# Kernel optimization log

Measured on AMD Instinct MI355X. Metric: run time of the kernel, lower is better.

Reference implementation:

```python
import jax, jax.numpy as jnp
import numpy as np

WS = 8        # window_size
SHIFT = 4     # shift_size
NH = 6        # num_heads
EPS = 1e-5


def _rel_pos_index(ws):
    coords = np.stack(np.meshgrid(np.arange(ws), np.arange(ws), indexing='ij'))  # [2,ws,ws]
    cf = coords.reshape(2, -1)                      # [2, ws*ws]
    rel = cf[:, :, None] - cf[:, None, :]           # [2, N, N]
    rel = rel.transpose(1, 2, 0)                    # [N, N, 2]
    rel[:, :, 0] += ws - 1
    rel[:, :, 1] += ws - 1
    rel[:, :, 0] *= 2 * ws - 1
    return rel.sum(-1)                              # [N, N] int


def _attn_mask(H, W, ws, shift):
    img = np.zeros((H, W), dtype=np.float32)
    slices = (slice(0, -ws), slice(-ws, -shift), slice(-shift, None))
    cnt = 0
    for hs in slices:
        for wsl in slices:
            img[hs, wsl] = cnt
            cnt += 1
    mw = img.reshape(H // ws, ws, W // ws, ws).transpose(0, 2, 1, 3).reshape(-1, ws * ws)
    diff = mw[:, None, :] - mw[:, :, None]          # [nW, N, N]
    return np.where(diff != 0, -100.0, 0.0).astype(np.float32)


def _layernorm(x, g, b):
    mu = x.mean(-1, keepdims=True)
    var = ((x - mu) ** 2).mean(-1, keepdims=True)
    return (x - mu) * jax.lax.rsqrt(var + EPS) * g + b


def setup_inputs() -> dict:
    key = jax.random.key(0)
    ks = jax.random.split(key, 8)
    C, HID = 192, 768
    return {
        'x': jax.random.normal(ks[0], (8, 128, 128, C), jnp.float32),
        'g1': jnp.ones((C,), jnp.float32),
        'b1': jnp.zeros((C,), jnp.float32),
        'qkv_w': jax.random.normal(ks[1], (3 * C, C), jnp.float32) * 0.02,
        'qkv_b': jnp.zeros((3 * C,), jnp.float32),
        'rpb_table': jax.random.normal(ks[2], ((2 * WS - 1) ** 2, NH), jnp.float32) * 0.02,
        'proj_w': jax.random.normal(ks[3], (C, C), jnp.float32) * 0.02,
        'proj_b': jnp.zeros((C,), jnp.float32),
        'g2': jnp.ones((C,), jnp.float32),
        'b2': jnp.zeros((C,), jnp.float32),
        'fc1_w': jax.random.normal(ks[4], (HID, C), jnp.float32) * 0.02,
        'fc1_b': jnp.zeros((HID,), jnp.float32),
        'fc2_w': jax.random.normal(ks[5], (C, HID), jnp.float32) * 0.02,
        'fc2_b': jnp.zeros((C,), jnp.float32),
    }


def reference(x, g1, b1, qkv_w, qkv_b, rpb_table, proj_w, proj_b, g2, b2,
              fc1_w, fc1_b, fc2_w, fc2_b):
    B, H, W, C = x.shape
    N = WS * WS
    hd = C // NH
    scale = hd ** -0.5

    rpi = jnp.asarray(_rel_pos_index(WS))                 # [N,N] static
    mask = jnp.asarray(_attn_mask(H, W, WS, SHIFT))       # [nW,N,N] static
    nW = mask.shape[0]

    shortcut = x.reshape(B, H * W, C)
    xn = _layernorm(shortcut, g1, b1).reshape(B, H, W, C)

    # cyclic shift
    xs = jnp.roll(xn, shift=(-SHIFT, -SHIFT), axis=(1, 2))

    # window partition -> [B*nW, N, C]
    win = xs.reshape(B, H // WS, WS, W // WS, WS, C).transpose(0, 1, 3, 2, 4, 5)
    win = win.reshape(-1, N, C)
    B_ = win.shape[0]

    # qkv
    qkv = jnp.einsum('bnc,oc->bno', win, qkv_w) + qkv_b   # [B_,N,3C]
    qkv = qkv.reshape(B_, N, 3, NH, hd).transpose(2, 0, 3, 1, 4)  # [3,B_,NH,N,hd]
    q, k, v = qkv[0] * scale, qkv[1], qkv[2]

    attn = jnp.einsum('bhnd,bhmd->bhnm', q, k)            # [B_,NH,N,N]
    bias = rpb_table[rpi.reshape(-1)].reshape(N, N, NH).transpose(2, 0, 1)
    attn = attn + bias[None]
    attn = attn.reshape(B, nW, NH, N, N) + mask[None, :, None]
    attn = jax.nn.softmax(attn.reshape(B_, NH, N, N), axis=-1)

    out = jnp.einsum('bhnm,bhmd->bhnd', attn, v)          # [B_,NH,N,hd]
    out = out.transpose(0, 2, 1, 3).reshape(B_, N, C)
    out = jnp.einsum('bnc,oc->bno', out, proj_w) + proj_b

    # window reverse -> [B,H,W,C]
    out = out.reshape(B, H // WS, W // WS, WS, WS, C).transpose(0, 1, 3, 2, 4, 5)
    out = out.reshape(B, H, W, C)
    out = jnp.roll(out, shift=(SHIFT, SHIFT), axis=(1, 2)).reshape(B, H * W, C)

    x1 = shortcut + out
    h = _layernorm(x1, g2, b2)
    h = jnp.einsum('bnc,hc->bnh', h, fc1_w) + fc1_b
    h = jax.nn.gelu(h, approximate=False)
    h = jnp.einsum('bnh,ch->bnc', h, fc2_w) + fc2_b
    x2 = x1 + h
    return x2.reshape(B, H, W, C)
```

## Files before the change

### kernel.cpp

```cpp
#include <hip/hip_runtime.h>
#include <hip/hip_bf16.h>

typedef __attribute__((ext_vector_type(8))) short s16x8;
typedef __attribute__((ext_vector_type(4))) float f32x4;

__device__ __forceinline__ unsigned short f2bf(float f){
    __hip_bfloat16 h = __float2bfloat16(f);
    return *reinterpret_cast<unsigned short*>(&h);
}

__device__ __forceinline__ int flab(int g){ return (g < 120) ? 0 : ((g < 124) ? 1 : 2); }

__device__ __forceinline__ void async16(const void* g, void* l){
    __builtin_amdgcn_global_load_lds(
        (const __attribute__((address_space(1))) unsigned int*)g,
        (__attribute__((address_space(3))) unsigned int*)l, 16, 0, 0);
}

__global__ __launch_bounds__(256) void wconv_all(
    const float* __restrict__ w0, const float* __restrict__ w1,
    const float* __restrict__ w2, const float* __restrict__ w3,
    unsigned short* __restrict__ o0, unsigned short* __restrict__ o1,
    unsigned short* __restrict__ o2, unsigned short* __restrict__ o3)
{
    int i = blockIdx.x*256 + threadIdx.x;
    if (i < 110592) o0[i] = f2bf(w0[i]);
    if (i < 36864)  o1[i] = f2bf(w1[i]);
    if (i < 147456) {
        int o = i/192, k = i - o*192;
        int oc = o/192, r = o - oc*192, ks = k>>5, c = k&31;
        o2[((oc*6 + ks)*192 + r)*32 + c] = f2bf(w2[i]);
    }
    if (i < 147456) {
        int o = i/768, k = i - o*768;
        int q = o/48, r = o - q*48, ks = k>>5, c = k&31;
        o3[((q*24 + ks)*48 + r)*32 + c] = f2bf(w3[i]);
    }
}

__global__ __launch_bounds__(256) void lnqkv_kernel(
    const float* __restrict__ x, const float* __restrict__ g1, const float* __restrict__ b1,
    const unsigned short* __restrict__ wq, const float* __restrict__ qkvb,
    unsigned short* __restrict__ qo, unsigned short* __restrict__ ko,
    unsigned short* __restrict__ vo)
{
    __shared__ __attribute__((aligned(16))) unsigned short win[64*200];
    __shared__ __attribute__((aligned(16))) unsigned short Bs[64*200];
    const int b_ = blockIdx.x;
    const int bb = b_>>8, wi = b_&255, wh = wi>>4, ww = wi&15;
    const int tid = threadIdx.x;
    const int wv = tid>>6, lane = tid&63, lrow = lane&15, quad = lane>>4;

    {
        const int n = tid>>2, q4 = tid&3;
        const int r = n>>3, c = n&7;
        const int hh = (wh*8 + r + 4)&127, wp = (ww*8 + c + 4)&127;
        const float* px = x + (((size_t)bb*128+hh)*128+wp)*192 + q4*48;
        float v[48];
        #pragma unroll
        for (int m=0;m<12;++m) *(float4*)(v+m*4) = *(const float4*)(px+m*4);
        float s = 0.f;
        #pragma unroll
        for (int k=0;k<48;++k) s += v[k];
        s += __shfl_xor(s,1); s += __shfl_xor(s,2);
        float mu = s*(1.0f/192.0f);
        float qv = 0.f;
        #pragma unroll
        for (int k=0;k<48;++k){ float d=v[k]-mu; qv += d*d; }
        qv += __shfl_xor(qv,1); qv += __shfl_xor(qv,2);
        float rstd = rsqrtf(qv*(1.0f/192.0f) + 1e-5f);
        const float* pg = g1 + q4*48;
        const float* pb = b1 + q4*48;
        unsigned short* pw = win + n*200 + q4*48;
        #pragma unroll
        for (int k=0;k<48;++k) pw[k] = f2bf((v[k]-mu)*rstd*pg[k] + pb[k]);
    }
    __syncthreads();

    s16x8 af[6];
    #pragma unroll
    for (int kc=0;kc<6;++kc)
        af[kc] = *(const s16x8*)(win + (wv*16+lrow)*200 + kc*32 + quad*8);

    for (int ot=0; ot<9; ++ot) {
        const int o0 = ot*64;
        __syncthreads();
        #pragma unroll
        for (int t=0;t<6;++t) {
            int cid = tid + t*256;
            *(int4*)(Bs + (cid/24)*200 + (cid%24)*8) =
                *(const int4*)(wq + (size_t)o0*192 + cid*8);
        }
        __syncthreads();
        f32x4 acc[4];
        #pragma unroll
        for (int j=0;j<4;++j) acc[j] = (f32x4){0.f,0.f,0.f,0.f};
        #pragma unroll
        for (int kc=0;kc<6;++kc)
            #pragma unroll
            for (int j=0;j<4;++j) {
                s16x8 bf = *(const s16x8*)(Bs + (j*16+lrow)*200 + kc*32 + quad*8);
                acc[j] = __builtin_amdgcn_mfma_f32_16x16x32_bf16(af[kc], bf, acc[j], 0, 0, 0);
            }
        __syncthreads();
        unsigned short* T = Bs;
        const int part = ot/3;
        float bv[4];
        #pragma unroll
        for (int j=0;j<4;++j) bv[j] = qkvb[o0 + j*16 + lrow];

        if (part < 2) {
            const float scale = (part==0) ? 0.17677669529663687f : 1.0f;
            #pragma unroll
            for (int j=0;j<4;++j)
                #pragma unroll
                for (int rg=0;rg<4;++rg) {
                    int n2 = wv*16 + quad*4 + rg;
                    T[n2*72 + j*16 + lrow] = f2bf((acc[j][rg]+bv[j])*scale);
                }
            __syncthreads();
            unsigned short* dst = (part==0) ? qo : ko;
            #pragma unroll
            for (int t=0;t<2;++t) {
                int c = tid + t*256;
                int n2 = c>>3, blk = c&7;
                int o_in = o0 + blk*8 - part*192;
                int head = o_in>>5, d = o_in&31;
                *(int4*)(dst + (((size_t)b_*6+head)*64 + n2)*32 + d) =
                    *(const int4*)(T + n2*72 + blk*8);
            }
        } else {
            #pragma unroll
            for (int j=0;j<4;++j)
                #pragma unroll
                for (int rg=0;rg<4;++rg) {
                    int n2 = wv*16 + quad*4 + rg;
                    T[(j*16+lrow)*72 + n2] = f2bf(acc[j][rg]+bv[j]);
                }
            __syncthreads();
            #pragma unroll
            for (int t=0;t<2;++t) {
                int c = tid + t*256;
                int ol = c>>3, nb = (c&7)*8;
                int o_in = o0 + ol - 384;
                int head = o_in>>5, d = o_in&31;
                *(int4*)(vo + (((size_t)b_*6+head)*32 + d)*64 + nb) =
                    *(const int4*)(T + ol*72 + nb);
            }
        }
    }
}

__global__ __launch_bounds__(384) void attn_kernel(
    const unsigned short* __restrict__ q, const unsigned short* __restrict__ k,
    const unsigned short* __restrict__ vT, const float* __restrict__ rpb,
    unsigned short* __restrict__ ao)
{
    __shared__ float rpb_s[1350];
    __shared__ __attribute__((aligned(16))) unsigned short p_lds[6*4608];
    const int b_ = blockIdx.x;
    const int h = threadIdx.x >> 6;
    const int lane = threadIdx.x & 63, lrow = lane & 15, quad = lane >> 4;
    for (int i = threadIdx.x; i < 1350; i += 384) rpb_s[i] = rpb[i];
    __syncthreads();

    const size_t hb = ((size_t)b_*6 + h)*2048;
    const unsigned short* qb = q  + hb;
    const unsigned short* kb = k  + hb;
    const unsigned short* vb = vT + hb;

    s16x8 qf[4], kf[4];
    #pragma unroll
    for (int i = 0; i < 4; ++i) qf[i] = *(const s16x8*)(qb + (i*16+lrow)*32 + quad*8);
    #pragma unroll
    for (int j = 0; j < 4; ++j) kf[j] = *(const s16x8*)(kb + (j*16+lrow)*32 + quad*8);

    const f32x4 zz = {0.f,0.f,0.f,0.f};
    f32x4 s[4][4];
    #pragma unroll
    for (int i = 0; i < 4; ++i)
        #pragma unroll
        for (int j = 0; j < 4; ++j)
            s[i][j] = __builtin_amdgcn_mfma_f32_16x16x32_bf16(qf[i], kf[j], zz, 0, 0, 0);

    const int wi = b_ & 255, wh = wi >> 4, ww = wi & 15;
    int labm[4];
    #pragma unroll
    for (int j = 0; j < 4; ++j) {
        int m = j*16 + lrow;
        labm[j] = flab(wh*8 + (m >> 3))*3 + flab(ww*8 + (m & 7));
    }
    unsigned short* pl = p_lds + h*4608;
    #pragma unroll
    for (int i = 0; i < 4; ++i) {
        #pragma unroll
        for (int rg = 0; rg < 4; ++rg) {
            int n = i*16 + quad*4 + rg;
            int rn = n >> 3, cn = n & 7;
            int labn = flab(wh*8 + rn)*3 + flab(ww*8 + cn);
            float vals[4];
            float vmax = -1e30f;
            #pragma unroll
            for (int j = 0; j < 4; ++j) {
                int m = j*16 + lrow;
                int idx = ((rn - (m >> 3) + 7)*15 + (cn - (m & 7) + 7))*6 + h;
                float val = s[i][j][rg] + rpb_s[idx];
                if (labn != labm[j]) val -= 100.f;
                vals[j] = val;
                vmax = fmaxf(vmax, val);
            }
            #pragma unroll
            for (int o = 1; o < 16; o <<= 1) vmax = fmaxf(vmax, __shfl_xor(vmax, o));
            float sum = 0.f;
            #pragma unroll
            for (int j = 0; j < 4; ++j) { vals[j] = __expf(vals[j] - vmax); sum += vals[j]; }
            #pragma unroll
            for (int o = 1; o < 16; o <<= 1) sum += __shfl_xor(sum, o);
            float inv = 1.f / sum;
            #pragma unroll
            for (int j = 0; j < 4; ++j) pl[n*72 + j*16 + lrow] = f2bf(vals[j]*inv);
        }
    }
    __syncthreads();

    f32x4 oacc[4][2];
    #pragma unroll
    for (int i = 0; i < 4; ++i) { oacc[i][0] = zz; oacc[i][1] = zz; }
    #pragma unroll
    for (int kc = 0; kc < 2; ++kc) {
        s16x8 vf[2];
        #pragma unroll
        for (int jd = 0; jd < 2; ++jd)
            vf[jd] = *(const s16x8*)(vb + (jd*16+lrow)*64 + kc*32 + quad*8);
        #pragma unroll
        for (int i = 0; i < 4; ++i) {
            s16x8 pf = *(const s16x8*)(pl + (i*16+lrow)*72 + kc*32 + quad*8);
            #pragma unroll
            for (int jd = 0; jd < 2; ++jd)
                oacc[i][jd] = __builtin_amdgcn_mfma_f32_16x16x32_bf16(pf, vf[jd], oacc[i][jd], 0, 0, 0);
        }
    }
    unsigned short* ob = ao + (size_t)b_*12288 + h*32;
    #pragma unroll
    for (int i = 0; i < 4; ++i)
        #pragma unroll
        for (int jd = 0; jd < 2; ++jd)
            #pragma unroll
            for (int rg = 0; rg < 4; ++rg) {
                int n = i*16 + quad*4 + rg;
                ob[(size_t)n*192 + jd*16 + lrow] = f2bf(oacc[i][jd][rg]);
            }
}

__device__ __forceinline__ void mm64x192(
    const unsigned short* __restrict__ A, const unsigned short* __restrict__ W,
    size_t m0, unsigned short* As, unsigned short* Bs, f32x4 (&acc)[12])
{
    const int tid = threadIdx.x, wv = tid>>6, lane = tid&63;
    const int lrow = lane&15, quad = lane>>4;
    const int grow = lane>>2;
    const int gcb  = (lane&3) ^ ((lane>>3)&3);
    #pragma unroll
    for (int j=0;j<12;++j) acc[j] = (f32x4){0.f,0.f,0.f,0.f};

    const unsigned short* Ab = A + (m0 + grow)*192 + gcb*8;
    const unsigned short* Wb = W + (size_t)grow*192 + gcb*8;

    auto issue = [&](int k0, unsigned short* Ad, unsigned short* Bd) {
        async16(Ab + (size_t)(wv*16)*192 + k0,     Ad + wv*512);
        async16(Wb + (size_t)(wv*16)*192 + k0,     Bd + wv*512);
        async16(Wb + (size_t)((wv+4)*16)*192 + k0, Bd + (wv+4)*512);
        async16(Wb + (size_t)((wv+8)*16)*192 + k0, Bd + (wv+8)*512);
    };
    issue(0, As, Bs);
    int cur = 0;
    for (int k0=0; k0<192; k0+=32) {
        __syncthreads();
        if (k0+32 < 192) issue(k0+32, As + (cur^1)*2048, Bs + (cur^1)*6144);
        const unsigned short* Ac = As + cur*2048;
        const unsigned short* Bc = Bs + cur*6144;
        const int rs = (quad ^ ((lrow>>1)&3)) << 3;
        s16x8 af = *(const s16x8*)(Ac + (wv*16+lrow)*32 + rs);
        #pragma unroll
        for (int j=0;j<12;++j) {
            s16x8 bf = *(const s16x8*)(Bc + (j*16+lrow)*32 + rs);
            acc[j] = __builtin_amdgcn_mfma_f32_16x16x32_bf16(af, bf, acc[j], 0, 0, 0);
        }
        cur ^= 1;
    }
}

__global__ __launch_bounds__(256) void projln_kernel(
    const unsigned short* __restrict__ A, const unsigned short* __restrict__ W,
    const float* __restrict__ pbias, const float* __restrict__ x,
    const float* __restrict__ g2, const float* __restrict__ b2,
    float* __restrict__ x1, unsigned short* __restrict__ xln2b)
{
    __shared__ __attribute__((aligned(16))) char smem[32768];
    unsigned short* As = (unsigned short*)smem;
    unsigned short* Bs = (unsigned short*)(smem + 8192);
    const int b_ = blockIdx.x;
    const int tid = threadIdx.x, wv = tid>>6, lane = tid&63;
    const int lrow = lane&15, quad = lane>>4;
    const size_t m0 = (size_t)b_*64;

    f32x4 acc[12];
    mm64x192(A, W, m0, As, Bs, acc);
    __syncthreads();

    const int bb = b_>>8, wi = b_&255, wh = wi>>4, ww = wi&15;
    float bv[12], gv[12], b2v[12];
    #pragma unroll
    for (int j=0;j<12;++j) {
        bv[j]  = pbias[j*16+lrow];
        gv[j]  = g2[j*16+lrow];
        b2v[j] = b2[j*16+lrow];
    }
    unsigned short* T = (unsigned short*)smem;
    #pragma unroll
    for (int rg=0;rg<4;++rg) {
        int n2 = wv*16 + quad*4 + rg;
        int r = n2>>3, c = n2&7;
        int hh = (wh*8+r+4)&127, wp = (ww*8+c+4)&127;
        size_t tok = ((size_t)bb*128+hh)*128 + wp;
        float xv[12];
        float s = 0.f;
        #pragma unroll
        for (int j=0;j<12;++j) {
            float t = acc[j][rg] + bv[j] + x[tok*192 + j*16 + lrow];
            xv[j] = t; s += t;
        }
        #pragma unroll
        for (int o=1;o<16;o<<=1) s += __shfl_xor(s, o);
        float mu = s*(1.0f/192.0f);
        float qv = 0.f;
        #pragma unroll
        for (int j=0;j<12;++j){ float d = xv[j]-mu; qv += d*d; }
        #pragma unroll
        for (int o=1;o<16;o<<=1) qv += __shfl_xor(qv, o);
        float rstd = rsqrtf(qv*(1.0f/192.0f) + 1e-5f);
        #pragma unroll
        for (int j=0;j<12;++j) {
            x1[tok*192 + j*16 + lrow] = xv[j];
            T[n2*200 + j*16 + lrow] = f2bf((xv[j]-mu)*rstd*gv[j] + b2v[j]);
        }
    }
    __syncthreads();
    #pragma unroll
    for (int t=0;t<6;++t) {
        int cid = tid + t*256;
        int n2 = cid/24, blk = cid%24;
        int r = n2>>3, c = n2&7;
        int hh = (wh*8+r+4)&127, wp = (ww*8+c+4)&127;
        size_t tok = ((size_t)bb*128+hh)*128 + wp;
        int row = (int)(tok & 127);
        int ks = blk>>2, kb = blk&3;
        int sw = (kb ^ ((row>>1)&3)) << 3;
        *(int4*)(xln2b + (tok>>7)*24576 + ks*4096 + row*32 + sw) =
            *(const int4*)(T + n2*200 + blk*8);
    }
}

__global__ __launch_bounds__(512, 4) void mlp_kernel(
    const unsigned short* __restrict__ Ablk,
    const unsigned short* __restrict__ W1b,
    const float* __restrict__ fc1b,
    const unsigned short* __restrict__ W2b,
    const float* __restrict__ fc2b,
    const float* __restrict__ x1, float* __restrict__ out)
{
    __shared__ __attribute__((aligned(16))) unsigned short Ald[6*2048];
    __shared__ __attribute__((aligned(16))) unsigned short Hld[6*2048];
    const int b_ = blockIdx.x;
    const int mt = b_>>1, half = b_&1;
    const int tid = threadIdx.x, wv = tid>>6, lane = tid&63;
    const int lrow = lane&15, quad = lane>>4;
    const int wr = wv>>2, wc = wv&3;
    const int r0 = wr*32, c0 = wc*48;
    const int rs = (quad ^ ((lrow>>1)&3)) << 3;

    {
        const unsigned short* src = Ablk + (size_t)mt*24576 + half*2048 + lane*8;
        #pragma unroll
        for (int r=0;r<3;++r) {
            int c = r*8 + wv;
            async16(src + (c>>2)*4096 + (c&3)*512, Ald + c*512);
        }
    }

    float bv1[4][3];
    #pragma unroll
    for (int oc=0;oc<4;++oc)
        #pragma unroll
        for (int j=0;j<3;++j) bv1[oc][j] = fc1b[oc*192 + c0 + j*16 + lrow];

    f32x4 a2[2][3];
    #pragma unroll
    for (int i=0;i<2;++i)
        #pragma unroll
        for (int j=0;j<3;++j) a2[i][j] = (f32x4){0.f,0.f,0.f,0.f};

    __syncthreads();

    for (int oc=0; oc<4; ++oc) {
        f32x4 a1[2][3];
        #pragma unroll
        for (int i=0;i<2;++i)
            #pragma unroll
            for (int j=0;j<3;++j) a1[i][j] = (f32x4){0.f,0.f,0.f,0.f};
        const unsigned short* w1p = W1b + (size_t)(oc*6)*6144 + (size_t)(c0)*32 + quad*8;
        #pragma unroll
        for (int ks=0;ks<6;++ks) {
            s16x8 af[2], bf[3];
            #pragma unroll
            for (int i=0;i<2;++i)
                af[i] = *(const s16x8*)(Ald + ks*2048 + (r0 + i*16 + lrow)*32 + rs);
            #pragma unroll
            for (int j=0;j<3;++j)
                bf[j] = *(const s16x8*)(w1p + (size_t)ks*6144 + (j*16 + lrow)*32);
            #pragma unroll
            for (int i=0;i<2;++i)
                #pragma unroll
                for (int j=0;j<3;++j)
                    a1[i][j] = __builtin_amdgcn_mfma_f32_16x16x32_bf16(af[i], bf[j], a1[i][j], 0, 0, 0);
        }

        if (oc) __syncthreads();

        #pragma unroll
        for (int i=0;i<2;++i)
            #pragma unroll
            for (int j=0;j<3;++j)
                #pragma unroll
                for (int rg=0;rg<4;++rg) {
                    int row = r0 + i*16 + quad*4 + rg;
                    int o = c0 + j*16 + lrow;
                    float v = a1[i][j][rg] + bv1[oc][j];
                    float v2 = v*v;
                    float z = v*(1.5957691216057308f + 0.07135481627f*v2);
                    float r = v * __builtin_amdgcn_rcpf(1.f + __expf(-z));
                    int ksh = o>>5, c5 = o&31;
                    Hld[ksh*2048 + row*32 + (((c5>>3) ^ ((row>>1)&3))<<3) + (c5&7)] = f2bf(r);
                }
        __syncthreads();

        const unsigned short* w2p = W2b + (size_t)(wc*24 + oc*6)*1536 + quad*8;
        #pragma unroll
        for (int ksl=0;ksl<6;++ksl) {
            s16x8 af2[2], bf2[3];
            #pragma unroll
            for (int i=0;i<2;++i)
                af2[i] = *(const s16x8*)(Hld + ksl*2048 + (r0 + i*16 + lrow)*32 + rs);
            #pragma unroll
            for (int j=0;j<3;++j)
                bf2[j] = *(const s16x8*)(w2p + (size_t)ksl*1536 + (j*16 + lrow)*32);
            #pragma unroll
            for (int i=0;i<2;++i)
                #pragma unroll
                for (int j=0;j<3;++j)
                    a2[i][j] = __builtin_amdgcn_mfma_f32_16x16x32_bf16(af2[i], bf2[j], a2[i][j], 0, 0, 0);
        }
    }

    {
        float bv2[3];
        #pragma unroll
        for (int j=0;j<3;++j) bv2[j] = fc2b[c0 + j*16 + lrow];
        #pragma unroll
        for (int i=0;i<2;++i)
            #pragma unroll
            for (int j=0;j<3;++j)
                #pragma unroll
                for (int rg=0;rg<4;++rg) {
                    size_t grow = (size_t)mt*128 + half*64 + r0 + i*16 + quad*4 + rg;
                    size_t ad = grow*192 + c0 + j*16 + lrow;
                    out[ad] = a2[i][j][rg] + bv2[j] + x1[ad];
                }
    }
}

extern "C" void kernel_launch(void* const* d_in, const int* in_sizes, int n_in,
                              void* d_out, int out_size, void* d_ws, size_t ws_size,
                              hipStream_t stream)
{
    const float* x      = (const float*)d_in[0];
    const float* g1     = (const float*)d_in[1];
    const float* b1     = (const float*)d_in[2];
    const float* qkv_w  = (const float*)d_in[3];
    const float* qkv_b  = (const float*)d_in[4];
    const float* rpb    = (const float*)d_in[5];
    const float* proj_w = (const float*)d_in[6];
    const float* proj_b = (const float*)d_in[7];
    const float* g2     = (const float*)d_in[8];
    const float* b2     = (const float*)d_in[9];
    const float* fc1_w  = (const float*)d_in[10];
    const float* fc1_b  = (const float*)d_in[11];
    const float* fc2_w  = (const float*)d_in[12];
    const float* fc2_b  = (const float*)d_in[13];
    float* out = (float*)d_out;
    char* ws = (char*)d_ws;

    if (ws_size < 353206272ULL) return;

    unsigned short* qbuf  = (unsigned short*)(ws + 0);
    unsigned short* kbuf  = (unsigned short*)(ws + 50331648);
    unsigned short* vbuf  = (unsigned short*)(ws + 100663296);
    unsigned short* attnO = (unsigned short*)(ws + 150994944);
    float*          x1    = (float*)        (ws + 201326592);
    unsigned short* xln2  = (unsigned short*)(ws + 301989888);
    unsigned short* wq    = (unsigned short*)(ws + 352321536);
    unsigned short* wp    = (unsigned short*)(ws + 352321536 + 221184);
    unsigned short* w1b   = (unsigned short*)(ws + 352321536 + 221184 + 73728);
    unsigned short* w2b   = (unsigned short*)(ws + 352321536 + 221184 + 73728 + 294912);

    wconv_all<<<576, 256, 0, stream>>>(qkv_w, proj_w, fc1_w, fc2_w, wq, wp, w1b, w2b);
    lnqkv_kernel<<<2048, 256, 0, stream>>>(x, g1, b1, wq, qkv_b, qbuf, kbuf, vbuf);
    attn_kernel<<<2048, 384, 0, stream>>>(qbuf, kbuf, vbuf, rpb, attnO);
    projln_kernel<<<2048, 256, 0, stream>>>(attnO, wp, proj_b, x, g2, b2, x1, xln2);
    mlp_kernel<<<2048, 512, 0, stream>>>(xln2, w1b, fc1_b, w2b, fc2_b, x1, out);
}
```

Baseline: 556.2 us.

## Fuse window attention with output projection and LayerNorm2 in one kernel

The attention kernel now keeps each window's attention output in LDS and runs the projection GEMM, residual add and second LayerNorm in the same block, so the separate projln kernel and the attnO round-trip through global memory are gone. The projection weights are streamed into LDS with double-buffered async loads while only 4 of the 6 waves do the MFMA work. Cost: two waves sit idle during the projection and epilogue, and launch bounds now request 3 blocks per CU, which may constrain registers.

```diff
diff --git a/kernel.cpp b/kernel.cpp
--- a/kernel.cpp
+++ b/kernel.cpp
@@ -151,17 +151,20 @@
     }
 }
 
-__global__ __launch_bounds__(384) void attn_kernel(
+__global__ __launch_bounds__(384, 3) void attnproj_kernel(
     const unsigned short* __restrict__ q, const unsigned short* __restrict__ k,
     const unsigned short* __restrict__ vT, const float* __restrict__ rpb,
-    unsigned short* __restrict__ ao)
+    const unsigned short* __restrict__ Wp, const float* __restrict__ pbias,
+    const float* __restrict__ x, const float* __restrict__ g2, const float* __restrict__ b2,
+    float* __restrict__ x1, unsigned short* __restrict__ xln2b)
 {
     __shared__ float rpb_s[1350];
-    __shared__ __attribute__((aligned(16))) unsigned short p_lds[6*4608];
+    __shared__ __attribute__((aligned(16))) unsigned short pool[6*4608];
     const int b_ = blockIdx.x;
-    const int h = threadIdx.x >> 6;
-    const int lane = threadIdx.x & 63, lrow = lane & 15, quad = lane >> 4;
-    for (int i = threadIdx.x; i < 1350; i += 384) rpb_s[i] = rpb[i];
+    const int tid = threadIdx.x;
+    const int h = tid >> 6;
+    const int lane = tid & 63, lrow = lane & 15, quad = lane >> 4;
+    for (int i = tid; i < 1350; i += 384) rpb_s[i] = rpb[i];
     __syncthreads();
 
     const size_t hb = ((size_t)b_*6 + h)*2048;
@@ -190,7 +193,7 @@
         int m = j*16 + lrow;
         labm[j] = flab(wh*8 + (m >> 3))*3 + flab(ww*8 + (m & 7));
     }
-    unsigned short* pl = p_lds + h*4608;
+    unsigned short* pl = pool + h*4608;
     #pragma unroll
     for (int i = 0; i < 4; ++i) {
         #pragma unroll
@@ -240,7 +243,10 @@
                 oacc[i][jd] = __builtin_amdgcn_mfma_f32_16x16x32_bf16(pf, vf[jd], oacc[i][jd], 0, 0, 0);
         }
     }
-    unsigned short* ob = ao + (size_t)b_*12288 + h*32;
+    __syncthreads();
+
+    unsigned short* Old = pool;
+    unsigned short* Bs  = pool + 12800;
     #pragma unroll
     for (int i = 0; i < 4; ++i)
         #pragma unroll
@@ -248,107 +254,80 @@
             #pragma unroll
             for (int rg = 0; rg < 4; ++rg) {
                 int n = i*16 + quad*4 + rg;
-                ob[(size_t)n*192 + jd*16 + lrow] = f2bf(oacc[i][jd][rg]);
-            }
-}
-
-__device__ __forceinline__ void mm64x192(
-    const unsigned short* __restrict__ A, const unsigned short* __restrict__ W,
-    size_t m0, unsigned short* As, unsigned short* Bs, f32x4 (&acc)[12])
-{
-    const int tid = threadIdx.x, wv = tid>>6, lane = tid&63;
-    const int lrow = lane&15, quad = lane>>4;
-    const int grow = lane>>2;
-    const int gcb  = (lane&3) ^ ((lane>>3)&3);
+                Old[n*200 + h*32 + jd*16 + lrow] = f2bf(oacc[i][jd][rg]);
+            }
+
+    const int grow = lane>>2, gcb = (lane&3)^((lane>>3)&3);
+    const unsigned short* Wb = Wp + (size_t)grow*192 + gcb*8;
+    auto stageB = [&](int k0, unsigned short* Bd) {
+        async16(Wb + (size_t)(h*16)*192 + k0,     Bd + h*512);
+        async16(Wb + (size_t)((h+6)*16)*192 + k0, Bd + (h+6)*512);
+    };
+    stageB(0, Bs);
+    __syncthreads();
+
+    f32x4 acc[12];
     #pragma unroll
     for (int j=0;j<12;++j) acc[j] = (f32x4){0.f,0.f,0.f,0.f};
-
-    const unsigned short* Ab = A + (m0 + grow)*192 + gcb*8;
-    const unsigned short* Wb = W + (size_t)grow*192 + gcb*8;
-
-    auto issue = [&](int k0, unsigned short* Ad, unsigned short* Bd) {
-        async16(Ab + (size_t)(wv*16)*192 + k0,     Ad + wv*512);
-        async16(Wb + (size_t)(wv*16)*192 + k0,     Bd + wv*512);
-        async16(Wb + (size_t)((wv+4)*16)*192 + k0, Bd + (wv+4)*512);
-        async16(Wb + (size_t)((wv+8)*16)*192 + k0, Bd + (wv+8)*512);
-    };
-    issue(0, As, Bs);
     int cur = 0;
-    for (int k0=0; k0<192; k0+=32) {
+    for (int kc=0; kc<6; ++kc) {
+        if (kc < 5) stageB((kc+1)*32, Bs + (cur^1)*6144);
+        if (h < 4) {
+            const int rs = (quad ^ ((lrow>>1)&3)) << 3;
+            s16x8 af = *(const s16x8*)(Old + (h*16+lrow)*200 + kc*32 + quad*8);
+            #pragma unroll
+            for (int j=0;j<12;++j) {
+                s16x8 bf = *(const s16x8*)(Bs + cur*6144 + (j*16+lrow)*32 + rs);
+                acc[j] = __builtin_amdgcn_mfma_f32_16x16x32_bf16(af, bf, acc[j], 0, 0, 0);
+            }
+        }
         __syncthreads();
-        if (k0+32 < 192) issue(k0+32, As + (cur^1)*2048, Bs + (cur^1)*6144);
-        const unsigned short* Ac = As + cur*2048;
-        const unsigned short* Bc = Bs + cur*6144;
-        const int rs = (quad ^ ((lrow>>1)&3)) << 3;
-        s16x8 af = *(const s16x8*)(Ac + (wv*16+lrow)*32 + rs);
+        cur ^= 1;
+    }
+
+    const int bb = b_>>8;
+    unsigned short* T = pool;
+    if (h < 4) {
+        float bv[12], gv[12], b2v[12];
         #pragma unroll
         for (int j=0;j<12;++j) {
-            s16x8 bf = *(const s16x8*)(Bc + (j*16+lrow)*32 + rs);
-            acc[j] = __builtin_amdgcn_mfma_f32_16x16x32_bf16(af, bf, acc[j], 0, 0, 0);
-        }
-        cur ^= 1;
-    }
-}
-
-__global__ __launch_bounds__(256) void projln_kernel(
-    const unsigned short* __restrict__ A, const unsigned short* __restrict__ W,
-    const float* __restrict__ pbias, const float* __restrict__ x,
-    const float* __restrict__ g2, const float* __restrict__ b2,
-    float* __restrict__ x1, unsigned short* __restrict__ xln2b)
-{
-    __shared__ __attribute__((aligned(16))) char smem[32768];
-    unsigned short* As = (unsigned short*)smem;
-    unsigned short* Bs = (unsigned short*)(smem + 8192);
-    const int b_ = blockIdx.x;
-    const int tid = threadIdx.x, wv = tid>>6, lane = tid&63;
-    const int lrow = lane&15, quad = lane>>4;
-    const size_t m0 = (size_t)b_*64;
-
-    f32x4 acc[12];
-    mm64x192(A, W, m0, As, Bs, acc);
-    __syncthreads();
-
-    const int bb = b_>>8, wi = b_&255, wh = wi>>4, ww = wi&15;
-    float bv[12], gv[12], b2v[12];
-    #pragma unroll
-    for (int j=0;j<12;++j) {
-        bv[j]  = pbias[j*16+lrow];
-        gv[j]  = g2[j*16+lrow];
-        b2v[j] = b2[j*16+lrow];
-    }
-    unsigned short* T = (unsigned short*)smem;
-    #pragma unroll
-    for (int rg=0;rg<4;++rg) {
-        int n2 = wv*16 + quad*4 + rg;
-        int r = n2>>3, c = n2&7;
-        int hh = (wh*8+r+4)&127, wp = (ww*8+c+4)&127;
-        size_t tok = ((size_t)bb*128+hh)*128 + wp;
-        float xv[12];
-        float s = 0.f;
-        #pragma unroll
-        for (int j=0;j<12;++j) {
-            float t = acc[j][rg] + bv[j] + x[tok*192 + j*16 + lrow];
-            xv[j] = t; s += t;
-        }
-        #pragma unroll
-        for (int o=1;o<16;o<<=1) s += __shfl_xor(s, o);
-        float mu = s*(1.0f/192.0f);
-        float qv = 0.f;
-        #pragma unroll
-        for (int j=0;j<12;++j){ float d = xv[j]-mu; qv += d*d; }
-        #pragma unroll
-        for (int o=1;o<16;o<<=1) qv += __shfl_xor(qv, o);
-        float rstd = rsqrtf(qv*(1.0f/192.0f) + 1e-5f);
-        #pragma unroll
-        for (int j=0;j<12;++j) {
-            x1[tok*192 + j*16 + lrow] = xv[j];
-            T[n2*200 + j*16 + lrow] = f2bf((xv[j]-mu)*rstd*gv[j] + b2v[j]);
-        }
-    }
-    __syncthreads();
-    #pragma unroll
-    for (int t=0;t<6;++t) {
-        int cid = tid + t*256;
+            bv[j]  = pbias[j*16+lrow];
+            gv[j]  = g2[j*16+lrow];
+            b2v[j] = b2[j*16+lrow];
+        }
+        #pragma unroll
+        for (int rg=0;rg<4;++rg) {
+            int n2 = h*16 + quad*4 + rg;
+            int r = n2>>3, c = n2&7;
+            int hh = (wh*8+r+4)&127, wp = (ww*8+c+4)&127;
+            size_t tok = ((size_t)bb*128+hh)*128 + wp;
+            float xv[12];
+            float sm = 0.f;
+            #pragma unroll
+            for (int j=0;j<12;++j) {
+                float t = acc[j][rg] + bv[j] + x[tok*192 + j*16 + lrow];
+                xv[j] = t; sm += t;
+            }
+            #pragma unroll
+            for (int o=1;o<16;o<<=1) sm += __shfl_xor(sm, o);
+            float mu = sm*(1.0f/192.0f);
+            float qv = 0.f;
+            #pragma unroll
+            for (int j=0;j<12;++j){ float d = xv[j]-mu; qv += d*d; }
+            #pragma unroll
+            for (int o=1;o<16;o<<=1) qv += __shfl_xor(qv, o);
+            float rstd = rsqrtf(qv*(1.0f/192.0f) + 1e-5f);
+            #pragma unroll
+            for (int j=0;j<12;++j) {
+                x1[tok*192 + j*16 + lrow] = xv[j];
+                T[n2*200 + j*16 + lrow] = f2bf((xv[j]-mu)*rstd*gv[j] + b2v[j]);
+            }
+        }
+    }
+    __syncthreads();
+    #pragma unroll
+    for (int t=0;t<4;++t) {
+        int cid = tid + t*384;
         int n2 = cid/24, blk = cid%24;
         int r = n2>>3, c = n2&7;
         int hh = (wh*8+r+4)&127, wp = (ww*8+c+4)&127;
@@ -505,7 +484,6 @@
     unsigned short* qbuf  = (unsigned short*)(ws + 0);
     unsigned short* kbuf  = (unsigned short*)(ws + 50331648);
     unsigned short* vbuf  = (unsigned short*)(ws + 100663296);
-    unsigned short* attnO = (unsigned short*)(ws + 150994944);
     float*          x1    = (float*)        (ws + 201326592);
     unsigned short* xln2  = (unsigned short*)(ws + 301989888);
     unsigned short* wq    = (unsigned short*)(ws + 352321536);
@@ -515,7 +493,7 @@
 
     wconv_all<<<576, 256, 0, stream>>>(qkv_w, proj_w, fc1_w, fc2_w, wq, wp, w1b, w2b);
     lnqkv_kernel<<<2048, 256, 0, stream>>>(x, g1, b1, wq, qkv_b, qbuf, kbuf, vbuf);
-    attn_kernel<<<2048, 384, 0, stream>>>(qbuf, kbuf, vbuf, rpb, attnO);
-    projln_kernel<<<2048, 256, 0, stream>>>(attnO, wp, proj_b, x, g2, b2, x1, xln2);
+    attnproj_kernel<<<2048, 384, 0, stream>>>(qbuf, kbuf, vbuf, rpb, wp, proj_b,
+                                              x, g2, b2, x1, xln2);
     mlp_kernel<<<2048, 512, 0, stream>>>(xln2, w1b, fc1_b, w2b, fc2_b, x1, out);
 }
```

Result: slower. 568.2 us (+2.1%).
